# Kernel tuning notes

Measured on AMD Instinct MI355X. Metric: run time of the kernel, lower is better.

The kernel has to match this reference:

```python
import jax, jax.numpy as jnp
import numpy as np

B, S, H, NH = 1, 2048, 768, 12
HD = H // NH  # 64


def setup_inputs() -> dict:
    key = jax.random.key(0)
    k0, k1, k2, k3 = jax.random.split(key, 4)
    BN = B * S
    return {
        "hidden_states": jax.random.normal(k0, (B, S, H), dtype=jnp.float32),
        "g": jax.random.uniform(k1, (BN, BN), dtype=jnp.float32),
        "attention_mask": jnp.zeros((B, S), dtype=jnp.float32),
        "Wq": jax.random.normal(k2, (H, H), dtype=jnp.float32) * 0.02,
        "bq": jnp.zeros((H,), dtype=jnp.float32),
        "Wv": jax.random.normal(k3, (H, H), dtype=jnp.float32) * 0.02,
        "bv": jnp.zeros((H,), dtype=jnp.float32),
    }


def reference(hidden_states, g, attention_mask, Wq, bq, Wv, bv):
    # hidden_states: [B, S, H] -> torch code transposes to [S, B, H]
    hs = jnp.swapaxes(hidden_states, 0, 1)  # [S, B, H]
    s, b, h = hs.shape
    BN = s * b

    q = hs @ Wq.T + bq  # [S, B, H]
    v = hs @ Wv.T + bv  # [S, B, H]

    # view(S,B,NH,HD).transpose(0,1) -> [B,S,NH,HD], then flat reshape to [NH, BN, HD]
    q = jnp.swapaxes(q.reshape(s, b, NH, HD), 0, 1).reshape(NH, BN, HD)
    # L2-normalize each query vector along head_dim (torch F.normalize, eps=1e-12)
    q = q / jnp.maximum(jnp.linalg.norm(q, axis=2, keepdims=True), 1e-12)

    # value: [B,S,NH,HD] flattened to [BN, NH, HD]
    v = jnp.swapaxes(v.reshape(s, b, NH, HD), 0, 1).reshape(BN, NH, HD)

    # attn sparsification mask combine (computed in original, but never used downstream)
    bool_mask = (attention_mask >= 0).reshape(-1, 1).astype(g.dtype)  # [BN, 1]
    _g_masked = g * (bool_mask @ bool_mask.T)  # dead value, kept for faithfulness

    # L2-distance attention scores: -(AA - 2AB + BB) / sqrt(head_dim)
    AB = jnp.einsum('hnd,hmd->hnm', q, q)            # [NH, BN, BN]
    AA = jnp.sum(q * q, axis=-1, keepdims=True)      # [NH, BN, 1]
    sim = -(AA - 2.0 * AB + jnp.swapaxes(AA, -1, -2)) * (HD ** -0.5)
    attn = jax.nn.softmax(sim, axis=-1)              # [NH, BN, BN]

    # weighted value sum: bmm(attn, v.transpose(0,1)) -> [NH, BN, HD]
    out = jnp.einsum('hnm,hmd->hnd', attn, jnp.swapaxes(v, 0, 1))

    # reshape(B,S,NH,HD) then merge last two dims -> [B, S, H]
    out = out.reshape(b, s, NH, HD).reshape(b, s, h)
    return out
```

## Files before the change

### kernel.cpp

```cpp
#include <hip/hip_runtime.h>
#include <math.h>

#define NTOK 2048
#define HDIM 768
#define NHEAD 12

typedef __attribute__((ext_vector_type(8))) short short8v;
typedef __attribute__((ext_vector_type(4))) float float4v;

static __device__ __forceinline__ unsigned short f2bf(float x) {
    unsigned u = __float_as_uint(x);
    return (unsigned short)((u + 0x7fffu + ((u >> 16) & 1u)) >> 16);
}

static __device__ __forceinline__ void gload_lds16(const void* g, void* lds_uniform) {
    __builtin_amdgcn_global_load_lds(
        (const __attribute__((address_space(1))) void*)g,
        (__attribute__((address_space(3))) void*)lds_uniform, 16, 0, 0);
}

__global__ __launch_bounds__(256) void cast_kernel(
    const float* __restrict__ hs, const float* __restrict__ Wq,
    const float* __restrict__ Wv, unsigned short* __restrict__ hsb,
    unsigned short* __restrict__ wqb, unsigned short* __restrict__ wvb)
{
    int gid = blockIdx.x * 256 + threadIdx.x;
    const float* src; unsigned short* dst; int off;
    if (gid < 393216)      { src = hs; dst = hsb; off = gid; }
    else if (gid < 540672) { src = Wq; dst = wqb; off = gid - 393216; }
    else                   { src = Wv; dst = wvb; off = gid - 540672; }
    float4 v = ((const float4*)src)[off];
    union { unsigned short u[4]; unsigned long long q; } pk;
    pk.u[0] = f2bf(v.x); pk.u[1] = f2bf(v.y);
    pk.u[2] = f2bf(v.z); pk.u[3] = f2bf(v.w);
    *(unsigned long long*)(dst + (size_t)off * 4) = pk.q;
}

__global__ __launch_bounds__(256) void projnorm_kernel(
    const unsigned short* __restrict__ hsb, const unsigned short* __restrict__ wqb,
    const unsigned short* __restrict__ wvb, const float* __restrict__ bq,
    const float* __restrict__ bv, unsigned short* __restrict__ qbf,
    unsigned short* __restrict__ vT)
{
    __shared__ unsigned short Asb[2][128 * 64];
    __shared__ unsigned short Bsb[2][64 * 64];

    const int tid = threadIdx.x, lane = tid & 63, w = tid >> 6;
    const int m0 = blockIdx.y * 128;
    const bool isq = (blockIdx.x < 12);
    const int n0 = (blockIdx.x % 12) * 64;
    const unsigned short* Wb = (isq ? wqb : wvb) + (size_t)n0 * HDIM;
    const float* bias = isq ? bq : bv;

#define STAGEP(buf, k0)                                                        \
    {                                                                          \
        _Pragma("unroll")                                                      \
        for (int i = 0; i < 4; ++i) {                  \
            int ci = ((w * 4 + i) << 6) + lane;                                \
            int r = ci >> 3, c8 = (ci & 7) ^ (r & 7);                          \
            gload_lds16(hsb + (size_t)(m0 + r) * HDIM + (k0) + (c8 << 3),      \
                        (char*)&Asb[buf][0] + ((w * 4 + i) << 10));            \
        }                                                                      \
        _Pragma("unroll")                                                      \
        for (int i = 0; i < 2; ++i) {                   \
            int ci = ((w * 2 + i) << 6) + lane;                                \
            int r = ci >> 3, c8 = (ci & 7) ^ (r & 7);                          \
            gload_lds16(Wb + (size_t)r * HDIM + (k0) + (c8 << 3),              \
                        (char*)&Bsb[buf][0] + ((w * 2 + i) << 10));            \
        }                                                                      \
    }

    float4v acc[2][4];
    #pragma unroll
    for (int fr = 0; fr < 2; ++fr)
        #pragma unroll
        for (int fc = 0; fc < 4; ++fc) acc[fr][fc] = (float4v){0.f, 0.f, 0.f, 0.f};

    STAGEP(0, 0);
    __syncthreads();

    for (int ks = 0; ks < 12; ++ks) {
        const int b = ks & 1;
        if (ks < 11) STAGEP(b ^ 1, (ks + 1) * 64);
        #pragma unroll
        for (int kk = 0; kk < 2; ++kk) {
            short8v af[2], bf[4];
            #pragma unroll
            for (int fr = 0; fr < 2; ++fr) {
                int row = w * 32 + fr * 16 + (lane & 15);
                int byt = ((row << 7) + (kk << 6) + ((lane >> 4) << 4)) ^ ((row & 7) << 4);
                af[fr] = *(const short8v*)((const char*)&Asb[b][0] + byt);
            }
            #pragma unroll
            for (int fc = 0; fc < 4; ++fc) {
                int row = fc * 16 + (lane & 15);
                int byt = ((row << 7) + (kk << 6) + ((lane >> 4) << 4)) ^ ((row & 7) << 4);
                bf[fc] = *(const short8v*)((const char*)&Bsb[b][0] + byt);
            }
            #pragma unroll
            for (int fr = 0; fr < 2; ++fr)
                #pragma unroll
                for (int fc = 0; fc < 4; ++fc)
                    acc[fr][fc] = __builtin_amdgcn_mfma_f32_16x16x32_bf16(
                        af[fr], bf[fc], acc[fr][fc], 0, 0, 0);
        }
        __syncthreads();
    }
#undef STAGEP

    float bcol[4];
    #pragma unroll
    for (int fc = 0; fc < 4; ++fc) bcol[fc] = bias[n0 + fc * 16 + (lane & 15)];

    if (isq) {
        #pragma unroll
        for (int fr = 0; fr < 2; ++fr)
            #pragma unroll
            for (int r = 0; r < 4; ++r) {
                float v[4];
                float ss = 0.f;
                #pragma unroll
                for (int fc = 0; fc < 4; ++fc) {
                    v[fc] = acc[fr][fc][r] + bcol[fc];
                    ss = fmaf(v[fc], v[fc], ss);
                }
                ss += __shfl_xor(ss, 1);
                ss += __shfl_xor(ss, 2);
                ss += __shfl_xor(ss, 4);
                ss += __shfl_xor(ss, 8);
                float inv = 1.0f / fmaxf(sqrtf(ss), 1e-12f);
                int m = m0 + w * 32 + fr * 16 + ((lane >> 4) << 2) + r;
                #pragma unroll
                for (int fc = 0; fc < 4; ++fc)
                    qbf[(size_t)m * HDIM + n0 + fc * 16 + (lane & 15)] = f2bf(v[fc] * inv);
            }
    } else {
        #pragma unroll
        for (int fr = 0; fr < 2; ++fr)
            #pragma unroll
            for (int fc = 0; fc < 4; ++fc) {
                int f = n0 + fc * 16 + (lane & 15);
                int mtk = m0 + w * 32 + fr * 16 + ((lane >> 4) << 2);
                union { unsigned short u[4]; unsigned long long q; } pk;
                #pragma unroll
                for (int r = 0; r < 4; ++r) pk.u[r] = f2bf(acc[fr][fc][r] + bcol[fc]);
                *(unsigned long long*)(vT + (size_t)f * NTOK + mtk) = pk.q;
            }
    }
}

__global__ __launch_bounds__(128) void attn_kernel(
    const unsigned short* __restrict__ qbf,
    const unsigned short* __restrict__ vT,
    float* __restrict__ out)
{
    __shared__ unsigned short Pl[2][16 * 72];

    const int bid = blockIdx.x;
    const int swz = (bid & 7) * 96 + (bid >> 3);
    const int h = swz >> 6, qt = swz & 63;
    const int tid = threadIdx.x, lane = tid & 63, w = tid >> 6;
    const int n0 = qt * 32 + w * 16;

    const unsigned short* kh = qbf + (size_t)h * NTOK * 64;
    const unsigned short* vh = vT + (size_t)h * 64 * NTOK;

    const unsigned short* qrow = kh + ((size_t)n0 + (lane & 15)) * 64;
    short8v qa[2];
    qa[0] = *(const short8v*)(qrow + ((lane >> 4) << 3));
    qa[1] = *(const short8v*)(qrow + 32 + ((lane >> 4) << 3));

    short8v kf[8], vf[8];
#define LOADK(mb)                                                              \
    _Pragma("unroll")                                                          \
    for (int t = 0; t < 4; ++t)                                                \
        _Pragma("unroll")                                                      \
        for (int kk = 0; kk < 2; ++kk)                                         \
            kf[t * 2 + kk] = *(const short8v*)(                                \
                kh + ((size_t)((mb) + t * 16 + (lane & 15))) * 64 +            \
                kk * 32 + ((lane >> 4) << 3));
#define LOADV(mb)                                                              \
    _Pragma("unroll")                                                          \
    for (int t = 0; t < 4; ++t)                                                \
        _Pragma("unroll")                                                      \
        for (int kk = 0; kk < 2; ++kk)                                         \
            vf[t * 2 + kk] = *(const short8v*)(                                \
                vh + (size_t)(t * 16 + (lane & 15)) * NTOK + (mb) +            \
                kk * 32 + ((lane >> 4) << 3));

    float4v acc[4];
    #pragma unroll
    for (int t = 0; t < 4; ++t) acc[t] = (float4v){0.f, 0.f, 0.f, 0.f};
    float lsum = 0.f;

    LOADK(0);
    LOADV(0);

    for (int mt = 0; mt < 32; ++mt) {
        float4v St[4];
        __builtin_amdgcn_s_setprio(1);
        #pragma unroll
        for (int t = 0; t < 4; ++t) {
            St[t] = (float4v){0.f, 0.f, 0.f, 0.f};
            St[t] = __builtin_amdgcn_mfma_f32_16x16x32_bf16(kf[t*2+0], qa[0], St[t], 0, 0, 0);
            St[t] = __builtin_amdgcn_mfma_f32_16x16x32_bf16(kf[t*2+1], qa[1], St[t], 0, 0, 0);
        }
        __builtin_amdgcn_s_setprio(0);

        if (mt < 31) LOADK((mt + 1) * 64);

        float p[4][4];
        float ls = 0.f;
        #pragma unroll
        for (int t = 0; t < 4; ++t)
            #pragma unroll
            for (int r = 0; r < 4; ++r) {
                p[t][r] = __expf(St[t][r] * 0.25f);
                ls += p[t][r];
            }
        ls += __shfl_xor(ls, 16);
        ls += __shfl_xor(ls, 32);
        lsum += ls;

        #pragma unroll
        for (int t = 0; t < 4; ++t) {
            unsigned w0, w1;
            asm volatile("v_cvt_pk_bf16_f32 %0, %1, %2"
                         : "=v"(w0) : "v"(p[t][0]), "v"(p[t][1]));
            asm volatile("v_cvt_pk_bf16_f32 %0, %1, %2"
                         : "=v"(w1) : "v"(p[t][2]), "v"(p[t][3]));
            unsigned long long q64 = (unsigned long long)w0 |
                                     ((unsigned long long)w1 << 32);
            *(unsigned long long*)(&Pl[w][(lane & 15) * 72 + t * 16 +
                                          ((lane >> 4) << 2)]) = q64;
        }
        asm volatile("s_waitcnt lgkmcnt(0)" ::: "memory");
        __builtin_amdgcn_sched_barrier(0);

        short8v pf[2];
        #pragma unroll
        for (int kk = 0; kk < 2; ++kk)
            pf[kk] = *(const short8v*)(&Pl[w][(lane & 15) * 72 + kk * 32 +
                                              ((lane >> 4) << 3)]);

        __builtin_amdgcn_s_setprio(1);
        #pragma unroll
        for (int t = 0; t < 4; ++t) {
            acc[t] = __builtin_amdgcn_mfma_f32_16x16x32_bf16(pf[0], vf[t*2+0], acc[t], 0, 0, 0);
            acc[t] = __builtin_amdgcn_mfma_f32_16x16x32_bf16(pf[1], vf[t*2+1], acc[t], 0, 0, 0);
        }
        __builtin_amdgcn_s_setprio(0);

        if (mt < 31) LOADV((mt + 1) * 64);
    }
#undef LOADK
#undef LOADV

    #pragma unroll
    for (int r = 0; r < 4; ++r) {
        float lv = __shfl(lsum, ((lane >> 4) << 2) + r);
        float inv = 1.0f / lv;
        int n = n0 + ((lane >> 4) << 2) + r;
        #pragma unroll
        for (int t = 0; t < 4; ++t)
            out[((size_t)h * NTOK + n) * 64 + t * 16 + (lane & 15)] = acc[t][r] * inv;
    }
}

extern "C" void kernel_launch(void* const* d_in, const int* in_sizes, int n_in,
                              void* d_out, int out_size, void* d_ws, size_t ws_size,
                              hipStream_t stream)
{
    const float* hs = (const float*)d_in[0];
    const float* Wq = (const float*)d_in[3];
    const float* bq = (const float*)d_in[4];
    const float* Wv = (const float*)d_in[5];
    const float* bv = (const float*)d_in[6];
    float* out = (float*)d_out;

    unsigned short* hsb = (unsigned short*)d_ws;
    unsigned short* wqb = hsb + (size_t)NTOK * HDIM;
    unsigned short* wvb = wqb + (size_t)HDIM * HDIM;
    unsigned short* qbf = wvb + (size_t)HDIM * HDIM;
    unsigned short* vT  = qbf + (size_t)NTOK * HDIM;

    cast_kernel<<<dim3(2688), 256, 0, stream>>>(hs, Wq, Wv, hsb, wqb, wvb);
    projnorm_kernel<<<dim3(24, 16), 256, 0, stream>>>(hsb, wqb, wvb, bq, bv, qbf, vT);
    attn_kernel<<<dim3(768), 128, 0, stream>>>(qbf, vT, out);
}
```

Before: 182.4 us.

## Fuse cast into projection and split attention keys across two blocks

Removes the separate bf16 cast kernel: the projection GEMM now loads fp32 inputs and weights, converts them in registers and writes them to padded LDS. The attention kernel splits the key range in two (split-K), doubling the block count, and stages K through swizzled shared memory with barriers. It writes unnormalised partial numerators and row sums, which a new combine kernel adds and normalises. This aims to raise occupancy and parallelism and cut a pass over memory, at the cost of extra partial-buffer traffic and one more launch.

```diff
diff --git a/kernel.cpp b/kernel.cpp
--- a/kernel.cpp
+++ b/kernel.cpp
@@ -4,6 +4,7 @@
 #define NTOK 2048
 #define HDIM 768
 #define NHEAD 12
+#define NQ (NTOK * NHEAD)
 
 typedef __attribute__((ext_vector_type(8))) short short8v;
 typedef __attribute__((ext_vector_type(4))) float float4v;
@@ -12,62 +13,57 @@
     unsigned u = __float_as_uint(x);
     return (unsigned short)((u + 0x7fffu + ((u >> 16) & 1u)) >> 16);
 }
-
+static __device__ __forceinline__ unsigned pk2(float a, float b) {
+    unsigned r;
+    asm("v_cvt_pk_bf16_f32 %0, %1, %2" : "=v"(r) : "v"(a), "v"(b));
+    return r;
+}
 static __device__ __forceinline__ void gload_lds16(const void* g, void* lds_uniform) {
     __builtin_amdgcn_global_load_lds(
         (const __attribute__((address_space(1))) void*)g,
         (__attribute__((address_space(3))) void*)lds_uniform, 16, 0, 0);
 }
 
-__global__ __launch_bounds__(256) void cast_kernel(
+__global__ __launch_bounds__(256) void projnorm_kernel(
     const float* __restrict__ hs, const float* __restrict__ Wq,
-    const float* __restrict__ Wv, unsigned short* __restrict__ hsb,
-    unsigned short* __restrict__ wqb, unsigned short* __restrict__ wvb)
-{
-    int gid = blockIdx.x * 256 + threadIdx.x;
-    const float* src; unsigned short* dst; int off;
-    if (gid < 393216)      { src = hs; dst = hsb; off = gid; }
-    else if (gid < 540672) { src = Wq; dst = wqb; off = gid - 393216; }
-    else                   { src = Wv; dst = wvb; off = gid - 540672; }
-    float4 v = ((const float4*)src)[off];
-    union { unsigned short u[4]; unsigned long long q; } pk;
-    pk.u[0] = f2bf(v.x); pk.u[1] = f2bf(v.y);
-    pk.u[2] = f2bf(v.z); pk.u[3] = f2bf(v.w);
-    *(unsigned long long*)(dst + (size_t)off * 4) = pk.q;
-}
-
-__global__ __launch_bounds__(256) void projnorm_kernel(
-    const unsigned short* __restrict__ hsb, const unsigned short* __restrict__ wqb,
-    const unsigned short* __restrict__ wvb, const float* __restrict__ bq,
+    const float* __restrict__ bq, const float* __restrict__ Wv,
     const float* __restrict__ bv, unsigned short* __restrict__ qbf,
     unsigned short* __restrict__ vT)
 {
-    __shared__ unsigned short Asb[2][128 * 64];
-    __shared__ unsigned short Bsb[2][64 * 64];
-
+    constexpr int PITCH = 40;
+    __shared__ unsigned short As[2][128 * PITCH];
+    __shared__ unsigned short Bs[2][64 * PITCH];
+
+    const bool isq = (blockIdx.z == 0);
+    const float* W    = isq ? Wq : Wv;
+    const float* bias = isq ? bq : bv;
+    const int n0 = blockIdx.x * 64, m0 = blockIdx.y * 128;
     const int tid = threadIdx.x, lane = tid & 63, w = tid >> 6;
-    const int m0 = blockIdx.y * 128;
-    const bool isq = (blockIdx.x < 12);
-    const int n0 = (blockIdx.x % 12) * 64;
-    const unsigned short* Wb = (isq ? wqb : wvb) + (size_t)n0 * HDIM;
-    const float* bias = isq ? bq : bv;
-
-#define STAGEP(buf, k0)                                                        \
+
+    const int arow = tid >> 1, acol = (tid & 1) * 16;
+    const int brow = tid >> 2, bcol = (tid & 3) * 8;
+    const float* ag = hs + (size_t)(m0 + arow) * HDIM + acol;
+    const float* bg = W + (size_t)(n0 + brow) * HDIM + bcol;
+
+    float4 ga[4], gb[2];
+#define PLOAD(k0)                                                              \
     {                                                                          \
-        _Pragma("unroll")                                                      \
-        for (int i = 0; i < 4; ++i) {                  \
-            int ci = ((w * 4 + i) << 6) + lane;                                \
-            int r = ci >> 3, c8 = (ci & 7) ^ (r & 7);                          \
-            gload_lds16(hsb + (size_t)(m0 + r) * HDIM + (k0) + (c8 << 3),      \
-                        (char*)&Asb[buf][0] + ((w * 4 + i) << 10));            \
-        }                                                                      \
-        _Pragma("unroll")                                                      \
-        for (int i = 0; i < 2; ++i) {                   \
-            int ci = ((w * 2 + i) << 6) + lane;                                \
-            int r = ci >> 3, c8 = (ci & 7) ^ (r & 7);                          \
-            gload_lds16(Wb + (size_t)r * HDIM + (k0) + (c8 << 3),              \
-                        (char*)&Bsb[buf][0] + ((w * 2 + i) << 10));            \
-        }                                                                      \
+        _Pragma("unroll") for (int i = 0; i < 4; ++i)                          \
+            ga[i] = *(const float4*)(ag + (k0) + i * 4);                       \
+        _Pragma("unroll") for (int i = 0; i < 2; ++i)                          \
+            gb[i] = *(const float4*)(bg + (k0) + i * 4);                       \
+    }
+#define PCVTW(b)                                                               \
+    {                                                                          \
+        uint4 u0 = {pk2(ga[0].x, ga[0].y), pk2(ga[0].z, ga[0].w),              \
+                    pk2(ga[1].x, ga[1].y), pk2(ga[1].z, ga[1].w)};             \
+        uint4 u1 = {pk2(ga[2].x, ga[2].y), pk2(ga[2].z, ga[2].w),              \
+                    pk2(ga[3].x, ga[3].y), pk2(ga[3].z, ga[3].w)};             \
+        *(uint4*)&As[b][arow * PITCH + acol]     = u0;                         \
+        *(uint4*)&As[b][arow * PITCH + acol + 8] = u1;                         \
+        uint4 u2 = {pk2(gb[0].x, gb[0].y), pk2(gb[0].z, gb[0].w),              \
+                    pk2(gb[1].x, gb[1].y), pk2(gb[1].z, gb[1].w)};             \
+        *(uint4*)&Bs[b][brow * PITCH + bcol] = u2;                             \
     }
 
     float4v acc[2][4];
@@ -76,41 +72,36 @@
         #pragma unroll
         for (int fc = 0; fc < 4; ++fc) acc[fr][fc] = (float4v){0.f, 0.f, 0.f, 0.f};
 
-    STAGEP(0, 0);
-    __syncthreads();
-
-    for (int ks = 0; ks < 12; ++ks) {
+    PLOAD(0);
+    PCVTW(0);
+
+    for (int ks = 0; ks < 24; ++ks) {
         const int b = ks & 1;
-        if (ks < 11) STAGEP(b ^ 1, (ks + 1) * 64);
-        #pragma unroll
-        for (int kk = 0; kk < 2; ++kk) {
-            short8v af[2], bf[4];
-            #pragma unroll
-            for (int fr = 0; fr < 2; ++fr) {
-                int row = w * 32 + fr * 16 + (lane & 15);
-                int byt = ((row << 7) + (kk << 6) + ((lane >> 4) << 4)) ^ ((row & 7) << 4);
-                af[fr] = *(const short8v*)((const char*)&Asb[b][0] + byt);
-            }
-            #pragma unroll
-            for (int fc = 0; fc < 4; ++fc) {
-                int row = fc * 16 + (lane & 15);
-                int byt = ((row << 7) + (kk << 6) + ((lane >> 4) << 4)) ^ ((row & 7) << 4);
-                bf[fc] = *(const short8v*)((const char*)&Bsb[b][0] + byt);
-            }
-            #pragma unroll
-            for (int fr = 0; fr < 2; ++fr)
-                #pragma unroll
-                for (int fc = 0; fc < 4; ++fc)
-                    acc[fr][fc] = __builtin_amdgcn_mfma_f32_16x16x32_bf16(
-                        af[fr], bf[fc], acc[fr][fc], 0, 0, 0);
-        }
+        if (ks < 23) PLOAD((ks + 1) * 32);
         __syncthreads();
-    }
-#undef STAGEP
-
-    float bcol[4];
+        short8v af[2], bf[4];
+        #pragma unroll
+        for (int fr = 0; fr < 2; ++fr)
+            af[fr] = *(const short8v*)
+                &As[b][(w * 32 + fr * 16 + (lane & 15)) * PITCH + ((lane >> 4) << 3)];
+        #pragma unroll
+        for (int fc = 0; fc < 4; ++fc)
+            bf[fc] = *(const short8v*)
+                &Bs[b][(fc * 16 + (lane & 15)) * PITCH + ((lane >> 4) << 3)];
+        #pragma unroll
+        for (int fr = 0; fr < 2; ++fr)
+            #pragma unroll
+            for (int fc = 0; fc < 4; ++fc)
+                acc[fr][fc] = __builtin_amdgcn_mfma_f32_16x16x32_bf16(
+                    af[fr], bf[fc], acc[fr][fc], 0, 0, 0);
+        if (ks < 23) PCVTW(b ^ 1);
+    }
+#undef PLOAD
+#undef PCVTW
+
+    float bcol4[4];
     #pragma unroll
-    for (int fc = 0; fc < 4; ++fc) bcol[fc] = bias[n0 + fc * 16 + (lane & 15)];
+    for (int fc = 0; fc < 4; ++fc) bcol4[fc] = bias[n0 + fc * 16 + (lane & 15)];
 
     if (isq) {
         #pragma unroll
@@ -121,7 +112,7 @@
                 float ss = 0.f;
                 #pragma unroll
                 for (int fc = 0; fc < 4; ++fc) {
-                    v[fc] = acc[fr][fc][r] + bcol[fc];
+                    v[fc] = acc[fr][fc][r] + bcol4[fc];
                     ss = fmaf(v[fc], v[fc], ss);
                 }
                 ss += __shfl_xor(ss, 1);
@@ -143,42 +134,49 @@
                 int mtk = m0 + w * 32 + fr * 16 + ((lane >> 4) << 2);
                 union { unsigned short u[4]; unsigned long long q; } pk;
                 #pragma unroll
-                for (int r = 0; r < 4; ++r) pk.u[r] = f2bf(acc[fr][fc][r] + bcol[fc]);
+                for (int r = 0; r < 4; ++r) pk.u[r] = f2bf(acc[fr][fc][r] + bcol4[fc]);
                 *(unsigned long long*)(vT + (size_t)f * NTOK + mtk) = pk.q;
             }
     }
 }
 
-__global__ __launch_bounds__(128) void attn_kernel(
+__global__ __launch_bounds__(128, 3) void attn_kernel(
     const unsigned short* __restrict__ qbf,
     const unsigned short* __restrict__ vT,
-    float* __restrict__ out)
+    float* __restrict__ num0,
+    float* __restrict__ part1,
+    float* __restrict__ lbuf)
 {
+    __shared__ unsigned short Ksb[2][64 * 64];
     __shared__ unsigned short Pl[2][16 * 72];
 
     const int bid = blockIdx.x;
-    const int swz = (bid & 7) * 96 + (bid >> 3);
-    const int h = swz >> 6, qt = swz & 63;
+    const int swz = (bid & 7) * 192 + (bid >> 3);
+    const int h = swz >> 7, rem = swz & 127;
+    const int qt = rem >> 1, ksp = rem & 1;
     const int tid = threadIdx.x, lane = tid & 63, w = tid >> 6;
-    const int n0 = qt * 32 + w * 16;
+    const int n0 = qt * 32;
+    const int kbase0 = ksp * 1024;
 
     const unsigned short* kh = qbf + (size_t)h * NTOK * 64;
     const unsigned short* vh = vT + (size_t)h * 64 * NTOK;
 
-    const unsigned short* qrow = kh + ((size_t)n0 + (lane & 15)) * 64;
+    const unsigned short* qrow = kh + ((size_t)n0 + w * 16 + (lane & 15)) * 64;
     short8v qa[2];
     qa[0] = *(const short8v*)(qrow + ((lane >> 4) << 3));
     qa[1] = *(const short8v*)(qrow + 32 + ((lane >> 4) << 3));
 
-    short8v kf[8], vf[8];
-#define LOADK(mb)                                                              \
-    _Pragma("unroll")                                                          \
-    for (int t = 0; t < 4; ++t)                                                \
+#define STAGE_K(buf, m0v)                                                      \
+    {                                                                          \
         _Pragma("unroll")                                                      \
-        for (int kk = 0; kk < 2; ++kk)                                         \
-            kf[t * 2 + kk] = *(const short8v*)(                                \
-                kh + ((size_t)((mb) + t * 16 + (lane & 15))) * 64 +            \
-                kk * 32 + ((lane >> 4) << 3));
+        for (int i = 0; i < 4; ++i) {           \
+            int ci = ((w * 4 + i) << 6) + lane;                                \
+            int r = ci >> 3, c8 = (ci & 7) ^ (r & 7);                          \
+            gload_lds16(kh + ((size_t)(m0v) + r) * 64 + (c8 << 3),             \
+                        (char*)&Ksb[buf][0] + ((w * 4 + i) << 10));            \
+        }                                                                      \
+    }
+    short8v vf[8];
 #define LOADV(mb)                                                              \
     _Pragma("unroll")                                                          \
     for (int t = 0; t < 4; ++t)                                                \
@@ -193,21 +191,28 @@
     for (int t = 0; t < 4; ++t) acc[t] = (float4v){0.f, 0.f, 0.f, 0.f};
     float lsum = 0.f;
 
-    LOADK(0);
-    LOADV(0);
-
-    for (int mt = 0; mt < 32; ++mt) {
+    STAGE_K(0, kbase0);
+    LOADV(kbase0);
+    __syncthreads();
+
+    for (int mt = 0; mt < 16; ++mt) {
+        const int cur = mt & 1;
+        if (mt < 15) STAGE_K(cur ^ 1, kbase0 + (mt + 1) * 64);
+
         float4v St[4];
         __builtin_amdgcn_s_setprio(1);
         #pragma unroll
         for (int t = 0; t < 4; ++t) {
             St[t] = (float4v){0.f, 0.f, 0.f, 0.f};
-            St[t] = __builtin_amdgcn_mfma_f32_16x16x32_bf16(kf[t*2+0], qa[0], St[t], 0, 0, 0);
-            St[t] = __builtin_amdgcn_mfma_f32_16x16x32_bf16(kf[t*2+1], qa[1], St[t], 0, 0, 0);
+            #pragma unroll
+            for (int kk = 0; kk < 2; ++kk) {
+                int row = (lane & 15) + (t << 4);
+                int off = ((row << 7) + (kk << 6) + ((lane >> 4) << 4)) ^ ((row & 7) << 4);
+                short8v kf = *(const short8v*)((const char*)&Ksb[cur][0] + off);
+                St[t] = __builtin_amdgcn_mfma_f32_16x16x32_bf16(kf, qa[kk], St[t], 0, 0, 0);
+            }
         }
         __builtin_amdgcn_s_setprio(0);
-
-        if (mt < 31) LOADK((mt + 1) * 64);
 
         float p[4][4];
         float ls = 0.f;
@@ -224,19 +229,15 @@
 
         #pragma unroll
         for (int t = 0; t < 4; ++t) {
-            unsigned w0, w1;
-            asm volatile("v_cvt_pk_bf16_f32 %0, %1, %2"
-                         : "=v"(w0) : "v"(p[t][0]), "v"(p[t][1]));
-            asm volatile("v_cvt_pk_bf16_f32 %0, %1, %2"
-                         : "=v"(w1) : "v"(p[t][2]), "v"(p[t][3]));
-            unsigned long long q64 = (unsigned long long)w0 |
-                                     ((unsigned long long)w1 << 32);
+            unsigned w0 = pk2(p[t][0], p[t][1]);
+            unsigned w1 = pk2(p[t][2], p[t][3]);
+            unsigned long long q64 =
+                (unsigned long long)w0 | ((unsigned long long)w1 << 32);
             *(unsigned long long*)(&Pl[w][(lane & 15) * 72 + t * 16 +
                                           ((lane >> 4) << 2)]) = q64;
         }
         asm volatile("s_waitcnt lgkmcnt(0)" ::: "memory");
         __builtin_amdgcn_sched_barrier(0);
-
         short8v pf[2];
         #pragma unroll
         for (int kk = 0; kk < 2; ++kk)
@@ -251,20 +252,41 @@
         }
         __builtin_amdgcn_s_setprio(0);
 
-        if (mt < 31) LOADV((mt + 1) * 64);
-    }
-#undef LOADK
+        if (mt < 15) {
+            LOADV(kbase0 + (mt + 1) * 64);
+            asm volatile("s_waitcnt vmcnt(8)" ::: "memory");
+            __builtin_amdgcn_s_barrier();
+            __builtin_amdgcn_sched_barrier(0);
+        }
+    }
+#undef STAGE_K
 #undef LOADV
 
+    float* nout = ksp ? part1 : num0;
     #pragma unroll
     for (int r = 0; r < 4; ++r) {
-        float lv = __shfl(lsum, ((lane >> 4) << 2) + r);
-        float inv = 1.0f / lv;
-        int n = n0 + ((lane >> 4) << 2) + r;
+        int n = n0 + w * 16 + ((lane >> 4) << 2) + r;
         #pragma unroll
         for (int t = 0; t < 4; ++t)
-            out[((size_t)h * NTOK + n) * 64 + t * 16 + (lane & 15)] = acc[t][r] * inv;
-    }
+            nout[((size_t)h * NTOK + n) * 64 + t * 16 + (lane & 15)] = acc[t][r];
+    }
+    if (lane < 16)
+        lbuf[ksp * NQ + h * NTOK + n0 + w * 16 + lane] = lsum;
+}
+
+__global__ __launch_bounds__(256) void combine_kernel(
+    float* __restrict__ out, const float* __restrict__ part1,
+    const float* __restrict__ lbuf)
+{
+    int gid = blockIdx.x * 256 + threadIdx.x;
+    float4 a = ((const float4*)out)[gid];
+    float4 b = ((const float4*)part1)[gid];
+    int row = gid >> 4;
+    float inv = 1.0f / (lbuf[row] + lbuf[NQ + row]);
+    float4 o;
+    o.x = (a.x + b.x) * inv; o.y = (a.y + b.y) * inv;
+    o.z = (a.z + b.z) * inv; o.w = (a.w + b.w) * inv;
+    ((float4*)out)[gid] = o;
 }
 
 extern "C" void kernel_launch(void* const* d_in, const int* in_sizes, int n_in,
@@ -278,13 +300,13 @@
     const float* bv = (const float*)d_in[6];
     float* out = (float*)d_out;
 
-    unsigned short* hsb = (unsigned short*)d_ws;
-    unsigned short* wqb = hsb + (size_t)NTOK * HDIM;
-    unsigned short* wvb = wqb + (size_t)HDIM * HDIM;
-    unsigned short* qbf = wvb + (size_t)HDIM * HDIM;
-    unsigned short* vT  = qbf + (size_t)NTOK * HDIM;
-
-    cast_kernel<<<dim3(2688), 256, 0, stream>>>(hs, Wq, Wv, hsb, wqb, wvb);
-    projnorm_kernel<<<dim3(24, 16), 256, 0, stream>>>(hsb, wqb, wvb, bq, bv, qbf, vT);
-    attn_kernel<<<dim3(768), 128, 0, stream>>>(qbf, vT, out);
-}
+    unsigned short* qbf   = (unsigned short*)d_ws;
+    unsigned short* vT    = qbf + (size_t)NTOK * HDIM;
+    float*          part1 = (float*)(vT + (size_t)HDIM * NTOK);
+    float*          lbuf  = part1 + (size_t)NQ * 64;
+
+    projnorm_kernel<<<dim3(12, 16, 2), 256, 0, stream>>>(
+        hs, Wq, bq, Wv, bv, qbf, vT);
+    attn_kernel<<<dim3(1536), 128, 0, stream>>>(qbf, vT, out, part1, lbuf);
+    combine_kernel<<<dim3(1536), 256, 0, stream>>>(out, part1, lbuf);
+}
```

After: 154.5 us. 1.18x faster.
